# Optimization experiments

Measured on AMD Instinct MI355X. Metric: run time of the kernel, lower is better.

The kernel has to match this reference:

```python
import jax, jax.numpy as jnp
import numpy as np

B, S, E = 8, 2048, 512

def setup_inputs() -> dict:
    key = jax.random.key(0)
    ks = jax.random.split(key, 7)
    Q = jax.random.normal(ks[0], (B, S, E), dtype=jnp.float32)
    K = jax.random.normal(ks[1], (B, S, E), dtype=jnp.float32)
    pad_mask = jax.random.randint(ks[2], (B, S, S), 0, 2).astype(bool)
    # torch nn.Linear weights are [out, in]; y = x @ W.T + b
    sc = 1.0 / np.sqrt(E)
    Wq = jax.random.uniform(ks[3], (E, E), jnp.float32, -sc, sc)
    Wk = jax.random.uniform(ks[4], (E, E), jnp.float32, -sc, sc)
    Wv = jax.random.uniform(ks[5], (E, E), jnp.float32, -sc, sc)
    Wp = jax.random.uniform(ks[6], (E, E), jnp.float32, -sc, sc)
    bp = jnp.zeros((E,), jnp.float32)
    return {"Q": Q, "K": K, "pad_mask": pad_mask, "Wq": Wq, "Wk": Wk, "Wv": Wv, "Wp": Wp, "bp": bp}

def reference(Q, K, pad_mask, Wq, Wk, Wv, Wp, bp):
    scale = E ** (-0.5)
    V = K  # V aliases K before projection, as in the original
    q = jnp.einsum('bse,fe->bsf', Q, Wq)   # q_map (no bias)
    k = jnp.einsum('bse,fe->bsf', K, Wk)   # k_map
    v = jnp.einsum('bse,fe->bsf', V, Wv)   # v_map
    scores = jnp.einsum('bqe,bke->bqk', q, k) * scale  # [B,S,S]
    scores = jnp.where(pad_mask, -1e9, scores)
    attn = jax.nn.softmax(scores, axis=-1)
    out = jnp.einsum('bqk,bke->bqe', attn, v)
    out = jnp.einsum('bse,fe->bsf', out, Wp) + bp       # proj
    return q + out  # residual uses projected Q (faithful to source)
```

## Files before the change

kernel.cpp:

```cpp
#include <hip/hip_runtime.h>
#include <hip/hip_bf16.h>

typedef short v8s __attribute__((ext_vector_type(8)));
typedef float v4f __attribute__((ext_vector_type(4)));

static constexpr int BB = 8, SS = 2048, EE = 512;

enum { EPI_BF16 = 0, EPI_SCALE = 1, EPI_FINAL = 2 };

struct EpiParams {
  float scale;
  const float* bias;
  const __hip_bfloat16* resid;
  int resid_ld;
};

static constexpr int SMEM_BYTES = 34816;

struct CastParams {
  const float* src[4];
  __hip_bfloat16* dst[4];
};

__global__ __launch_bounds__(256) void cast_weights(CastParams cp) {
  const int seg = blockIdx.x >> 7;
  const int b = blockIdx.x & 127;
  const float* x = cp.src[seg] + (unsigned long long)b * 2048;
  __hip_bfloat16* y = cp.dst[seg] + (unsigned long long)b * 2048;
  int i = threadIdx.x * 8;
  float4 f0 = ((const float4*)(x + i))[0];
  float4 f1 = ((const float4*)(x + i))[1];
  alignas(16) __hip_bfloat16 h[8];
  h[0] = __float2bfloat16(f0.x); h[1] = __float2bfloat16(f0.y);
  h[2] = __float2bfloat16(f0.z); h[3] = __float2bfloat16(f0.w);
  h[4] = __float2bfloat16(f1.x); h[5] = __float2bfloat16(f1.y);
  h[6] = __float2bfloat16(f1.z); h[7] = __float2bfloat16(f1.w);
  *(uint4*)(y + i) = *(uint4*)h;
}

__device__ __forceinline__ void stage_tile64(const __hip_bfloat16* __restrict__ G,
                                             int row0, int ld, int k0,
                                             __hip_bfloat16* lds, int wave, int lane) {
#pragma unroll
  for (int t = 0; t < 4; ++t) {
    const int p = (wave * 4 + t) * 64 + lane;
    const int row = p >> 3;
    const int g = (p & 7) ^ (row & 7);
    const __hip_bfloat16* src = G + (unsigned long long)(row0 + row) * ld + k0 + g * 8;
    __builtin_amdgcn_global_load_lds(
        (const __attribute__((address_space(1))) void*)src,
        (__attribute__((address_space(3))) void*)(lds + (wave * 4 + t) * 512),
        16, 0, 0);
  }
}

__device__ __forceinline__ void stage_tile64_f32(const float* __restrict__ G,
                                                 int row0, int ld, int k0,
                                                 __hip_bfloat16* lds, int tid) {
#pragma unroll
  for (int c = 0; c < 4; ++c) {
    const int p = c * 256 + tid;
    const int row = p >> 3;
    const int g = (p & 7) ^ (row & 7);
    const float* src = G + (unsigned long long)(row0 + row) * ld + k0 + g * 8;
    float4 f0 = ((const float4*)src)[0];
    float4 f1 = ((const float4*)src)[1];
    alignas(16) __hip_bfloat16 h[8];
    h[0] = __float2bfloat16(f0.x); h[1] = __float2bfloat16(f0.y);
    h[2] = __float2bfloat16(f0.z); h[3] = __float2bfloat16(f0.w);
    h[4] = __float2bfloat16(f1.x); h[5] = __float2bfloat16(f1.y);
    h[6] = __float2bfloat16(f1.z); h[7] = __float2bfloat16(f1.w);
    *(uint4*)&lds[p * 8] = *(uint4*)h;
  }
}

template <int EPI, bool AF32, bool BF32>
__device__ __forceinline__ void gemm_body(const void* Agv, const void* Bgv,
                                          void* Cg, int K, int lda, int ldb, int ldc,
                                          int m0, int n0, const EpiParams& ep,
                                          unsigned char* smem) {
  __hip_bfloat16* As = (__hip_bfloat16*)smem;
  __hip_bfloat16* Bs = As + 128 * 64;

  const int tid = threadIdx.x;
  const int lane = tid & 63;
  const int wave = tid >> 6;
  const int wr = wave >> 1;
  const int wc = wave & 1;

  v4f acc[4][4];
  const v4f vzero = {0.f, 0.f, 0.f, 0.f};
#pragma unroll
  for (int i = 0; i < 4; ++i)
#pragma unroll
    for (int j = 0; j < 4; ++j) acc[i][j] = vzero;

  const int fr = lane & 15;
  const int fq = lane >> 4;

  for (int k0 = 0; k0 < K; k0 += 64) {
    __syncthreads();
    if constexpr (AF32)
      stage_tile64_f32((const float*)Agv, m0, lda, k0, As, tid);
    else
      stage_tile64((const __hip_bfloat16*)Agv, m0, lda, k0, As, wave, lane);
    if constexpr (BF32)
      stage_tile64_f32((const float*)Bgv, n0, ldb, k0, Bs, tid);
    else
      stage_tile64((const __hip_bfloat16*)Bgv, n0, ldb, k0, Bs, wave, lane);
    __syncthreads();

#pragma unroll
    for (int ks = 0; ks < 2; ++ks) {
      const int gq = ks * 4 + fq;
      v8s a[4], b[4];
#pragma unroll
      for (int i = 0; i < 4; ++i) {
        const int r = wr * 64 + i * 16 + fr;
        a[i] = *(const v8s*)&As[r * 64 + ((gq ^ (r & 7)) * 8)];
      }
#pragma unroll
      for (int j = 0; j < 4; ++j) {
        const int r = wc * 64 + j * 16 + fr;
        b[j] = *(const v8s*)&Bs[r * 64 + ((gq ^ (r & 7)) * 8)];
      }
#pragma unroll
      for (int i = 0; i < 4; ++i)
#pragma unroll
        for (int j = 0; j < 4; ++j)
          acc[i][j] = __builtin_amdgcn_mfma_f32_16x16x32_bf16(a[i], b[j], acc[i][j], 0, 0, 0);
    }
  }

  const int cf = lane & 15;
  const int rq = (lane >> 4) * 4;

  __syncthreads();

  if constexpr (EPI != EPI_FINAL) {
    __hip_bfloat16* Ct = (__hip_bfloat16*)smem;
    const int ST = 136;
#pragma unroll
    for (int i = 0; i < 4; ++i) {
      const int rl = wr * 64 + i * 16 + rq;
#pragma unroll
      for (int j = 0; j < 4; ++j) {
        const int col = wc * 64 + j * 16 + cf;
#pragma unroll
        for (int r = 0; r < 4; ++r) {
          float v = acc[i][j][r];
          if constexpr (EPI == EPI_SCALE) v *= ep.scale;
          Ct[(rl + r) * ST + col] = __float2bfloat16(v);
        }
      }
    }
    __syncthreads();
    __hip_bfloat16* C = (__hip_bfloat16*)Cg;
#pragma unroll
    for (int c = 0; c < 8; ++c) {
      const int idx = c * 256 + tid;
      const int row = idx >> 4;
      const int colc = (idx & 15) * 8;
      *(v8s*)&C[(unsigned long long)(m0 + row) * ldc + n0 + colc] =
          *(const v8s*)&Ct[row * ST + colc];
    }
  } else {
    float* Cf = (float*)smem;
    const int ST = 132;
    float* C = (float*)Cg;
#pragma unroll
    for (int h = 0; h < 2; ++h) {
      if (wr == h) {
#pragma unroll
        for (int i = 0; i < 4; ++i) {
          const int rl = i * 16 + rq;
#pragma unroll
          for (int j = 0; j < 4; ++j) {
            const int col = wc * 64 + j * 16 + cf;
#pragma unroll
            for (int r = 0; r < 4; ++r) Cf[(rl + r) * ST + col] = acc[i][j][r];
          }
        }
      }
      __syncthreads();
#pragma unroll
      for (int c = 0; c < 8; ++c) {
        const int idx = c * 256 + tid;
        const int row = idx >> 5;
        const int colc = (idx & 31) * 4;
        const int grow = m0 + h * 64 + row;
        const int gcol = n0 + colc;
        float4 v = *(const float4*)&Cf[row * ST + colc];
        float4 b4 = *(const float4*)&ep.bias[gcol];
        ushort4 r4 = *(const ushort4*)&ep.resid[(unsigned long long)grow * ep.resid_ld + gcol];
        v.x += b4.x + __bfloat162float(*(__hip_bfloat16*)&r4.x);
        v.y += b4.y + __bfloat162float(*(__hip_bfloat16*)&r4.y);
        v.z += b4.z + __bfloat162float(*(__hip_bfloat16*)&r4.z);
        v.w += b4.w + __bfloat162float(*(__hip_bfloat16*)&r4.w);
        *(float4*)&C[(unsigned long long)grow * ldc + gcol] = v;
      }
      if (h == 0) __syncthreads();
    }
  }
}

template <int EPI>
__global__ __launch_bounds__(256, 3) void gemm_bt(
    const __hip_bfloat16* __restrict__ Ag, const __hip_bfloat16* __restrict__ Bg,
    void* __restrict__ Cg, int K, int lda, int ldb, int ldc,
    unsigned long long sAz, unsigned long long sBz, unsigned long long sCz, EpiParams ep) {
  __shared__ __align__(16) unsigned char smem[SMEM_BYTES];
  const unsigned long long z = blockIdx.z;
  void* Cz;
  if constexpr (EPI == EPI_FINAL) Cz = (void*)((float*)Cg + z * sCz);
  else Cz = (void*)((__hip_bfloat16*)Cg + z * sCz);
  gemm_body<EPI, false, false>(Ag + z * sAz, Bg + z * sBz, Cz, K, lda, ldb, ldc,
                               blockIdx.y * 128, blockIdx.x * 128, ep, smem);
}

__global__ __launch_bounds__(256, 3) void gemm_qkv(
    const float* __restrict__ Q, const float* __restrict__ K,
    const __hip_bfloat16* __restrict__ Wq, const __hip_bfloat16* __restrict__ Wk,
    const __hip_bfloat16* __restrict__ Wv,
    __hip_bfloat16* __restrict__ qb, __hip_bfloat16* __restrict__ kb,
    __hip_bfloat16* __restrict__ vT) {
  __shared__ __align__(16) unsigned char smem[SMEM_BYTES];
  const int z = blockIdx.z;
  EpiParams ep{};
  if (z == 2) {
    gemm_body<EPI_BF16, false, true>(Wv, K, vT, EE, EE, EE, BB * SS,
                                     blockIdx.y * 128, blockIdx.x * 128, ep, smem);
  } else {
    const float* A = (z == 0) ? Q : K;
    const __hip_bfloat16* B = (z == 0) ? Wq : Wk;
    __hip_bfloat16* C = (z == 0) ? qb : kb;
    gemm_body<EPI_BF16, true, false>(A, B, C, EE, EE, EE, EE,
                                     blockIdx.x * 128, blockIdx.y * 128, ep, smem);
  }
}

__global__ __launch_bounds__(256) void softmax_rows(__hip_bfloat16* __restrict__ sc,
                                                    const unsigned char* __restrict__ mask) {
  const unsigned long long row = blockIdx.x;
  __hip_bfloat16* p = sc + row * (unsigned long long)SS;
  const int tid = threadIdx.x;
  const int lane = tid & 63;
  const int wv = tid >> 6;

  alignas(16) __hip_bfloat16 hv[8];
  ((uint4*)hv)[0] = *(const uint4*)&p[tid * 8];
  const unsigned long long mbits =
      *(const unsigned long long*)(mask + row * (unsigned long long)SS + tid * 8);

  float v[8];
  float m = -3.4e38f;
#pragma unroll
  for (int i = 0; i < 8; ++i) {
    v[i] = ((mbits >> (8 * i)) & 0xffull) ? -1e9f : __bfloat162float(hv[i]);
    m = fmaxf(m, v[i]);
  }
#pragma unroll
  for (int off = 32; off >= 1; off >>= 1) m = fmaxf(m, __shfl_xor(m, off));

  __shared__ float redm[4];
  __shared__ float reds[4];
  if (lane == 0) redm[wv] = m;
  __syncthreads();
  m = fmaxf(fmaxf(redm[0], redm[1]), fmaxf(redm[2], redm[3]));

  float s = 0.f;
#pragma unroll
  for (int i = 0; i < 8; ++i) {
    v[i] = __expf(v[i] - m);
    s += v[i];
  }
#pragma unroll
  for (int off = 32; off >= 1; off >>= 1) s += __shfl_xor(s, off);
  if (lane == 0) reds[wv] = s;
  __syncthreads();
  s = reds[0] + reds[1] + reds[2] + reds[3];
  const float inv = 1.0f / s;

#pragma unroll
  for (int i = 0; i < 8; ++i) hv[i] = __float2bfloat16(v[i] * inv);
  *(uint4*)&p[tid * 8] = ((uint4*)hv)[0];
}

extern "C" void kernel_launch(void* const* d_in, const int* in_sizes, int n_in,
                              void* d_out, int out_size, void* d_ws, size_t ws_size,
                              hipStream_t stream) {
  const float* Q = (const float*)d_in[0];
  const float* K = (const float*)d_in[1];
  const unsigned char* mask = (const unsigned char*)d_in[2];
  const float* Wq = (const float*)d_in[3];
  const float* Wk = (const float*)d_in[4];
  const float* Wv = (const float*)d_in[5];
  const float* Wp = (const float*)d_in[6];
  const float* bp = (const float*)d_in[7];
  float* out = (float*)d_out;

  char* ws = (char*)d_ws;
  const unsigned long long MB = 1024ull * 1024ull;
  __hip_bfloat16* qb = (__hip_bfloat16*)(ws + 0 * MB);
  __hip_bfloat16* kb = (__hip_bfloat16*)(ws + 16 * MB);
  __hip_bfloat16* ob = kb;
  __hip_bfloat16* vT = (__hip_bfloat16*)(ws + 32 * MB);
  __hip_bfloat16* Wqb = (__hip_bfloat16*)(ws + 48 * MB);
  __hip_bfloat16* Wkb = Wqb + 512 * 512;
  __hip_bfloat16* Wvb = Wkb + 512 * 512;
  __hip_bfloat16* Wpb = Wvb + 512 * 512;
  __hip_bfloat16* sc = (__hip_bfloat16*)(ws + 64 * MB);

  dim3 blk(256, 1, 1);

  CastParams cp;
  cp.src[0] = Wq; cp.dst[0] = Wqb;
  cp.src[1] = Wk; cp.dst[1] = Wkb;
  cp.src[2] = Wv; cp.dst[2] = Wvb;
  cp.src[3] = Wp; cp.dst[3] = Wpb;
  cast_weights<<<dim3(512, 1, 1), blk, 0, stream>>>(cp);

  gemm_qkv<<<dim3((BB * SS) / 128, EE / 128, 3), blk, 0, stream>>>(
      Q, K, Wqb, Wkb, Wvb, qb, kb, vT);

  EpiParams eps{};
  eps.scale = 0.044194173824159216f;
  gemm_bt<EPI_SCALE><<<dim3(SS / 128, SS / 128, BB), blk, 0, stream>>>(
      qb, kb, sc, EE, EE, EE, SS,
      (unsigned long long)SS * EE, (unsigned long long)SS * EE,
      (unsigned long long)SS * SS, eps);

  softmax_rows<<<dim3(BB * SS, 1, 1), blk, 0, stream>>>(sc, mask);

  EpiParams ep0{};
  gemm_bt<EPI_BF16><<<dim3(EE / 128, SS / 128, BB), blk, 0, stream>>>(
      sc, vT, ob, SS, SS, BB * SS, EE,
      (unsigned long long)SS * SS, (unsigned long long)SS,
      (unsigned long long)SS * EE, ep0);

  EpiParams epf{};
  epf.bias = bp;
  epf.resid = qb;
  epf.resid_ld = EE;
  gemm_bt<EPI_FINAL><<<dim3(EE / 128, (BB * SS) / 128, 1), blk, 0, stream>>>(
      ob, Wpb, out, EE, EE, EE, EE, 0ull, 0ull, 0ull, epf);
}
```

Measured before the change: 380.0 us.

## Fuse QK^T, masked softmax and PV into a single flash-attention kernel

Replaces the score GEMM, row softmax and PV GEMM with one kernel that computes attention per 64-query tile using an online softmax. K tiles are double-buffered in LDS via global_load_lds, probabilities go through LDS to feed the PV MFMAs, and V^T is read directly from global memory. This avoids materializing and re-reading the full bf16 score matrix. In exchange it uses a large LDS footprint, launches only 256 blocks, and adds several block-wide barriers per KV step, which could limit occupancy.

Result: slower. 413.1 us (+8.7%).

```diff
diff --git a/kernel.cpp b/kernel.cpp
--- a/kernel.cpp
+++ b/kernel.cpp
@@ -239,51 +239,192 @@
   }
 }
 
-__global__ __launch_bounds__(256) void softmax_rows(__hip_bfloat16* __restrict__ sc,
-                                                    const unsigned char* __restrict__ mask) {
-  const unsigned long long row = blockIdx.x;
-  __hip_bfloat16* p = sc + row * (unsigned long long)SS;
+static constexpr int FLASH_LDS = 149248;
+
+__device__ __forceinline__ void stage_K64(const __hip_bfloat16* __restrict__ Kb, int kv0,
+                                          __hip_bfloat16* lds, int tid) {
+  const int wv = tid >> 6;
+#pragma unroll
+  for (int c = 0; c < 8; ++c) {
+    const int p = c * 512 + tid;
+    const int chunk = p >> 9;
+    const int row = (p >> 3) & 63;
+    const int g = (p & 7) ^ (row & 7);
+    const __hip_bfloat16* src = Kb + (unsigned long long)(kv0 + row) * 512ull + chunk * 64 + g * 8;
+    __builtin_amdgcn_global_load_lds(
+        (const __attribute__((address_space(1))) void*)src,
+        (__attribute__((address_space(3))) void*)(lds + (c * 512 + wv * 64) * 8),
+        16, 0, 0);
+  }
+}
+
+__global__ __launch_bounds__(512, 2) void flash_attn(
+    const __hip_bfloat16* __restrict__ qb, const __hip_bfloat16* __restrict__ kb,
+    const __hip_bfloat16* __restrict__ vT, const unsigned char* __restrict__ mask,
+    __hip_bfloat16* __restrict__ ob) {
+  extern __shared__ __align__(16) char fsm[];
+  __hip_bfloat16* Ks0 = (__hip_bfloat16*)fsm;
+  __hip_bfloat16* Ps0 = Ks0 + 2 * 32768;
+  float* m_s   = (float*)(fsm + 147456);
+  float* l_s   = m_s + 64;
+  float* fac_s = l_s + 64;
+  float* pmax  = fac_s + 64;
+  float* psum  = pmax + 128;
+
   const int tid = threadIdx.x;
   const int lane = tid & 63;
-  const int wv = tid >> 6;
-
-  alignas(16) __hip_bfloat16 hv[8];
-  ((uint4*)hv)[0] = *(const uint4*)&p[tid * 8];
-  const unsigned long long mbits =
-      *(const unsigned long long*)(mask + row * (unsigned long long)SS + tid * 8);
-
-  float v[8];
-  float m = -3.4e38f;
-#pragma unroll
-  for (int i = 0; i < 8; ++i) {
-    v[i] = ((mbits >> (8 * i)) & 0xffull) ? -1e9f : __bfloat162float(hv[i]);
-    m = fmaxf(m, v[i]);
-  }
-#pragma unroll
-  for (int off = 32; off >= 1; off >>= 1) m = fmaxf(m, __shfl_xor(m, off));
-
-  __shared__ float redm[4];
-  __shared__ float reds[4];
-  if (lane == 0) redm[wv] = m;
+  const int w = tid >> 6;
+  const int fr = lane & 15;
+  const int fq = lane >> 4;
+  const int wq = w & 3;
+  const int wk = w >> 2;
+  const int b = blockIdx.x & 7;
+  const int q0 = (blockIdx.x >> 3) * 64;
+  const unsigned long long bS = (unsigned long long)b * 2048ull;
+  const float SC = 0.044194173824159216f;
+
+  v8s qf[16];
+  {
+    const __hip_bfloat16* qrow = qb + (bS + q0 + wq * 16 + fr) * 512ull;
+#pragma unroll
+    for (int kk = 0; kk < 16; ++kk) qf[kk] = *(const v8s*)&qrow[kk * 32 + fq * 8];
+  }
+
+  v4f acc[4][4];
+  const v4f vz = {0.f, 0.f, 0.f, 0.f};
+#pragma unroll
+  for (int i = 0; i < 4; ++i)
+#pragma unroll
+    for (int j = 0; j < 4; ++j) acc[i][j] = vz;
+
+  if (tid < 64) { m_s[tid] = -1e30f; l_s[tid] = 0.f; }
+
+  const __hip_bfloat16* Kb = kb + bS * 512ull;
+  stage_K64(Kb, 0, Ks0, tid);
   __syncthreads();
-  m = fmaxf(fmaxf(redm[0], redm[1]), fmaxf(redm[2], redm[3]));
-
-  float s = 0.f;
-#pragma unroll
-  for (int i = 0; i < 8; ++i) {
-    v[i] = __expf(v[i] - m);
-    s += v[i];
-  }
-#pragma unroll
-  for (int off = 32; off >= 1; off >>= 1) s += __shfl_xor(s, off);
-  if (lane == 0) reds[wv] = s;
+
+  for (int t = 0; t < 32; ++t) {
+    __hip_bfloat16* KsT = Ks0 + (t & 1) * 32768;
+    __hip_bfloat16* PsT = Ps0 + (t & 1) * 4096;
+    if (t < 31) stage_K64(Kb, (t + 1) * 64, Ks0 + ((t + 1) & 1) * 32768, tid);
+
+    const int kv0 = t * 64;
+
+    unsigned char mk[2][4];
+#pragma unroll
+    for (int j = 0; j < 2; ++j)
+#pragma unroll
+      for (int r = 0; r < 4; ++r)
+        mk[j][r] = mask[(bS + q0 + wq * 16 + fq * 4 + r) * 2048ull + kv0 + wk * 32 + j * 16 + fr];
+
+    v4f sa[2] = {vz, vz};
+    __builtin_amdgcn_s_setprio(1);
+#pragma unroll
+    for (int kk = 0; kk < 16; ++kk) {
+#pragma unroll
+      for (int j = 0; j < 2; ++j) {
+        const int rr = wk * 32 + j * 16 + fr;
+        v8s kf = *(const v8s*)&KsT[(kk >> 1) * 4096 + rr * 64 + ((((kk & 1) * 4 + fq) ^ (rr & 7)) * 8)];
+        sa[j] = __builtin_amdgcn_mfma_f32_16x16x32_bf16(qf[kk], kf, sa[j], 0, 0, 0);
+      }
+    }
+    __builtin_amdgcn_s_setprio(0);
+
+    float sv[2][4];
+    float rmx[4] = {-3e38f, -3e38f, -3e38f, -3e38f};
+#pragma unroll
+    for (int j = 0; j < 2; ++j)
+#pragma unroll
+      for (int r = 0; r < 4; ++r) {
+        const float x = mk[j][r] ? -1e9f : sa[j][r] * SC;
+        sv[j][r] = x;
+        rmx[r] = fmaxf(rmx[r], x);
+      }
+#pragma unroll
+    for (int off = 1; off <= 8; off <<= 1)
+#pragma unroll
+      for (int r = 0; r < 4; ++r) rmx[r] = fmaxf(rmx[r], __shfl_xor(rmx[r], off));
+    if (fr == 0)
+      *(float4*)&pmax[wk * 64 + wq * 16 + fq * 4] = make_float4(rmx[0], rmx[1], rmx[2], rmx[3]);
+    __syncthreads();
+
+    if (tid < 64) {
+      const float mo = m_s[tid];
+      const float mn = fmaxf(mo, fmaxf(pmax[tid], pmax[64 + tid]));
+      m_s[tid] = mn;
+      fac_s[tid] = __expf(mo - mn);
+    }
+    __syncthreads();
+
+    float4 mn4 = *(const float4*)&m_s[wq * 16 + fq * 4];
+    const float mnr[4] = {mn4.x, mn4.y, mn4.z, mn4.w};
+    float rsm[4] = {0.f, 0.f, 0.f, 0.f};
+#pragma unroll
+    for (int j = 0; j < 2; ++j) {
+      const int col = wk * 32 + j * 16 + fr;
+      const int cg = col >> 3, cl = col & 7;
+#pragma unroll
+      for (int r = 0; r < 4; ++r) {
+        const float p = __expf(sv[j][r] - mnr[r]);
+        rsm[r] += p;
+        const int row = wq * 16 + fq * 4 + r;
+        PsT[row * 64 + ((cg ^ (row & 7)) * 8) + cl] = __float2bfloat16(p);
+      }
+    }
+#pragma unroll
+    for (int off = 1; off <= 8; off <<= 1)
+#pragma unroll
+      for (int r = 0; r < 4; ++r) rsm[r] += __shfl_xor(rsm[r], off);
+    if (fr == 0)
+      *(float4*)&psum[wk * 64 + wq * 16 + fq * 4] = make_float4(rsm[0], rsm[1], rsm[2], rsm[3]);
+#pragma unroll
+    for (int i = 0; i < 4; ++i) {
+      const float4 f4 = *(const float4*)&fac_s[i * 16 + fq * 4];
+      const float fv[4] = {f4.x, f4.y, f4.z, f4.w};
+#pragma unroll
+      for (int j = 0; j < 4; ++j)
+#pragma unroll
+        for (int r = 0; r < 4; ++r) acc[i][j][r] *= fv[r];
+    }
+    __syncthreads();
+
+    if (tid < 64) l_s[tid] = l_s[tid] * fac_s[tid] + psum[tid] + psum[64 + tid];
+
+    __builtin_amdgcn_s_setprio(1);
+#pragma unroll
+    for (int ks = 0; ks < 2; ++ks) {
+      v8s pa[4], vb[4];
+#pragma unroll
+      for (int i = 0; i < 4; ++i) {
+        const int row = i * 16 + fr;
+        pa[i] = *(const v8s*)&PsT[row * 64 + (((ks * 4 + fq) ^ (row & 7)) * 8)];
+      }
+#pragma unroll
+      for (int j = 0; j < 4; ++j)
+        vb[j] = *(const v8s*)&vT[(unsigned long long)(w * 64 + j * 16 + fr) * 16384ull +
+                                 bS + kv0 + ks * 32 + fq * 8];
+#pragma unroll
+      for (int i = 0; i < 4; ++i)
+#pragma unroll
+        for (int j = 0; j < 4; ++j)
+          acc[i][j] = __builtin_amdgcn_mfma_f32_16x16x32_bf16(pa[i], vb[j], acc[i][j], 0, 0, 0);
+    }
+    __builtin_amdgcn_s_setprio(0);
+  }
+
   __syncthreads();
-  s = reds[0] + reds[1] + reds[2] + reds[3];
-  const float inv = 1.0f / s;
-
-#pragma unroll
-  for (int i = 0; i < 8; ++i) hv[i] = __float2bfloat16(v[i] * inv);
-  *(uint4*)&p[tid * 8] = ((uint4*)hv)[0];
+#pragma unroll
+  for (int i = 0; i < 4; ++i) {
+    const float4 l4 = *(const float4*)&l_s[i * 16 + fq * 4];
+    const float inv[4] = {1.f / l4.x, 1.f / l4.y, 1.f / l4.z, 1.f / l4.w};
+#pragma unroll
+    for (int r = 0; r < 4; ++r) {
+      __hip_bfloat16* orow = ob + (bS + q0 + i * 16 + fq * 4 + r) * 512ull + w * 64 + fr;
+#pragma unroll
+      for (int j = 0; j < 4; ++j)
+        orow[j * 16] = __float2bfloat16(acc[i][j][r] * inv[r]);
+    }
+  }
 }
 
 extern "C" void kernel_launch(void* const* d_in, const int* in_sizes, int n_in,
@@ -303,13 +444,12 @@
   const unsigned long long MB = 1024ull * 1024ull;
   __hip_bfloat16* qb = (__hip_bfloat16*)(ws + 0 * MB);
   __hip_bfloat16* kb = (__hip_bfloat16*)(ws + 16 * MB);
-  __hip_bfloat16* ob = kb;
   __hip_bfloat16* vT = (__hip_bfloat16*)(ws + 32 * MB);
   __hip_bfloat16* Wqb = (__hip_bfloat16*)(ws + 48 * MB);
   __hip_bfloat16* Wkb = Wqb + 512 * 512;
   __hip_bfloat16* Wvb = Wkb + 512 * 512;
   __hip_bfloat16* Wpb = Wvb + 512 * 512;
-  __hip_bfloat16* sc = (__hip_bfloat16*)(ws + 64 * MB);
+  __hip_bfloat16* ob = (__hip_bfloat16*)(ws + 64 * MB);
 
   dim3 blk(256, 1, 1);
 
@@ -323,20 +463,14 @@
   gemm_qkv<<<dim3((BB * SS) / 128, EE / 128, 3), blk, 0, stream>>>(
       Q, K, Wqb, Wkb, Wvb, qb, kb, vT);
 
-  EpiParams eps{};
-  eps.scale = 0.044194173824159216f;
-  gemm_bt<EPI_SCALE><<<dim3(SS / 128, SS / 128, BB), blk, 0, stream>>>(
-      qb, kb, sc, EE, EE, EE, SS,
-      (unsigned long long)SS * EE, (unsigned long long)SS * EE,
-      (unsigned long long)SS * SS, eps);
-
-  softmax_rows<<<dim3(BB * SS, 1, 1), blk, 0, stream>>>(sc, mask);
-
-  EpiParams ep0{};
-  gemm_bt<EPI_BF16><<<dim3(EE / 128, SS / 128, BB), blk, 0, stream>>>(
-      sc, vT, ob, SS, SS, BB * SS, EE,
-      (unsigned long long)SS * SS, (unsigned long long)SS,
-      (unsigned long long)SS * EE, ep0);
+  static bool attr_done = false;
+  if (!attr_done) {
+    hipFuncSetAttribute((const void*)flash_attn,
+                        hipFuncAttributeMaxDynamicSharedMemorySize, FLASH_LDS);
+    attr_done = true;
+  }
+  flash_attn<<<dim3(256, 1, 1), dim3(512, 1, 1), FLASH_LDS, stream>>>(
+      qb, kb, vT, mask, ob);
 
   EpiParams epf{};
   epf.bias = bp;
```
